# Kernel tuning notes

Hardware: AMD Instinct MI355X
Metric: run time of the kernel (lower is better)

## Reference

```python
import jax, jax.numpy as jnp
import numpy as np

N = 50000      # nodes
E = 800000     # edges (avg degree 16)
D = 128        # in_dim = hidden_dim
C = 40         # num_classes
BN_EPS = 1e-5


def setup_inputs() -> dict:
    key = jax.random.key(0)
    ks = jax.random.split(key, 24)
    h = jax.random.normal(ks[0], (N, D), dtype=jnp.float32)
    edge_src = jax.random.randint(ks[1], (E,), 0, N)
    edge_dst = jax.random.randint(ks[2], (E,), 0, N)
    mask = jnp.ones((E, 1), dtype=jnp.float32)  # adj_mask2_fixed (frozen)

    def lin_w(k, fi, fo):
        return jax.random.normal(k, (fi, fo), dtype=jnp.float32) / np.sqrt(fi).astype(np.float32)

    def lin_b(k, fo):
        return jax.random.normal(k, (fo,), dtype=jnp.float32) * 0.01

    dims = [(D, D), (D, D), (D, C)]  # last GIN layer -> num_classes
    out = {"h": h, "edge_src": edge_src, "edge_dst": edge_dst, "mask": mask}
    for i, (fi, fo) in enumerate(dims):
        out[f"w{i}"] = lin_w(ks[3 + 4 * i], fi, fo)
        out[f"b{i}"] = lin_b(ks[4 + 4 * i], fo)
        out[f"g{i}"] = jnp.ones((fo,), jnp.float32) + 0.05 * jax.random.normal(ks[5 + 4 * i], (fo,), jnp.float32)
        out[f"beta{i}"] = 0.05 * jax.random.normal(ks[6 + 4 * i], (fo,), jnp.float32)
        out[f"rm{i}"] = 0.1 * jax.random.normal(jax.random.fold_in(key, 100 + i), (fo,), jnp.float32)
        out[f"rv{i}"] = jax.random.uniform(jax.random.fold_in(key, 200 + i), (fo,), jnp.float32, 0.5, 1.5)
    out["wp"] = lin_w(ks[20], D, C)
    out["bp"] = lin_b(ks[21], C)
    return out


def reference(h, edge_src, edge_dst, mask,
              w0, b0, g0, beta0, rm0, rv0,
              w1, b1, g1, beta1, rm1, rv1,
              w2, b2, g2, beta2, rm2, rv2,
              wp, bp):
    # in-degree for mean aggregation (DGL mean reducer: divide by in-degree,
    # zero for isolated nodes)
    ones_e = jnp.ones(edge_dst.shape, dtype=h.dtype)
    deg = jax.ops.segment_sum(ones_e, edge_dst, num_segments=N)
    deg_inv = jnp.where(deg > 0, 1.0 / jnp.maximum(deg, 1.0), 0.0)[:, None]

    def gin_layer(x, w, b, g, beta, rm, rv):
        msg = x[edge_src] * mask                                   # [E, d]
        agg = jax.ops.segment_sum(msg, edge_dst, num_segments=N) * deg_inv
        z = (x + agg) @ w + b                                      # (1+eps)=1, eps=0
        z = (z - rm) * jax.lax.rsqrt(rv + BN_EPS) * g + beta       # BN (eval, running stats)
        return jax.nn.relu(z)                                      # dropout: eval -> identity

    h1 = gin_layer(h, w0, b0, g0, beta0, rm0, rv0)    # [N, D]
    h2 = gin_layer(h1, w1, b1, g1, beta1, rm1, rv1)   # [N, D]  hidden_rep[-2]
    h3 = gin_layer(h2, w2, b2, g2, beta2, rm2, rv2)   # [N, C]  hidden_rep[-1]
    return ((h2 @ wp + bp) + h3) * 0.5
```

## Files before the change

### kernel.cpp

```cpp
#include <hip/hip_runtime.h>

#define N_NODES 50000
#define N_EDGES 800000
#define DIM 128
#define NCLS 40

#define NCHUNK 128
#define CE 6250
#define HALF_N 25088
#define WHALF 12544
#define SCAN_B 98
#define N_PAD 50432

typedef __bf16 bf16x8_t __attribute__((ext_vector_type(8)));
typedef unsigned short us8_t __attribute__((ext_vector_type(8)));
typedef float f32x4_t __attribute__((ext_vector_type(4)));

static __device__ __forceinline__ float b2f(unsigned short h) {
    unsigned u = ((unsigned)h) << 16;
    return __builtin_bit_cast(float, u);
}
static __device__ __forceinline__ unsigned short f2b(float f) {
    unsigned u = __builtin_bit_cast(unsigned, f);
    u += 0x7FFFu + ((u >> 16) & 1u);
    return (unsigned short)(u >> 16);
}

__global__ __launch_bounds__(256) void to_bf16(const float* __restrict__ in,
                                               unsigned short* __restrict__ out) {
    size_t e0 = ((size_t)blockIdx.x * 256 + threadIdx.x) * 8;
    f32x4_t v0 = *(const f32x4_t*)(in + e0);
    f32x4_t v1 = *(const f32x4_t*)(in + e0 + 4);
    us8_t o;
    #pragma unroll
    for (int j = 0; j < 4; ++j) { o[j] = f2b(v0[j]); o[4 + j] = f2b(v1[j]); }
    *(us8_t*)(out + e0) = o;
}

__global__ __launch_bounds__(256) void repack_w(const float* __restrict__ w0,
                                                const float* __restrict__ w1,
                                                const float* __restrict__ w2,
                                                const float* __restrict__ wp,
                                                unsigned short* __restrict__ f0h,
                                                unsigned short* __restrict__ f0l,
                                                unsigned short* __restrict__ f1h,
                                                unsigned short* __restrict__ f1l,
                                                unsigned short* __restrict__ f2h,
                                                unsigned short* __restrict__ f2l,
                                                unsigned short* __restrict__ fph,
                                                unsigned short* __restrict__ fpl) {
    int t = blockIdx.x * 256 + threadIdx.x;
    const float* src;
    unsigned short *dh, *dl;
    int idx, ncols;
    if (t < 16384)      { src = w0; dh = f0h; dl = f0l; idx = t;         ncols = 128; }
    else if (t < 32768) { src = w1; dh = f1h; dl = f1l; idx = t - 16384; ncols = 128; }
    else if (t < 38912) { src = w2; dh = f2h; dl = f2l; idx = t - 32768; ncols = 48; }
    else if (t < 45056) { src = wp; dh = fph; dl = fpl; idx = t - 38912; ncols = 48; }
    else return;
    int k = idx / ncols, n = idx - k * ncols;
    float v;
    if (ncols == 128) v = src[k * 128 + n];
    else              v = (n < NCLS) ? src[k * NCLS + n] : 0.f;
    int nt = n >> 4, m = n & 15, kt = k >> 5, quad = (k >> 3) & 3, j = k & 7;
    int off = ((nt * 4 + kt) * 64 + quad * 16 + m) * 8 + j;
    unsigned short hi = f2b(v);
    dh[off] = hi;
    dl[off] = f2b(v - b2f(hi));
}

__global__ __launch_bounds__(256) void chunk_count(const int* __restrict__ dst,
                                                   unsigned* __restrict__ cnt) {
    __shared__ unsigned lds[WHALF];
    int c = blockIdx.x, h = blockIdx.y, tid = threadIdx.x;
    for (int w = tid; w < WHALF; w += 256) lds[w] = 0;
    __syncthreads();
    int base = c * CE;
    for (int k = tid; k < CE; k += 256) {
        int local = dst[base + k] - h * HALF_N;
        if (local >= 0 && local < HALF_N)
            atomicAdd(&lds[local >> 1], 1u << ((local & 1) * 16));
    }
    __syncthreads();
    unsigned* out = cnt + ((size_t)(h * NCHUNK + c)) * WHALF;
    for (int w = tid; w < WHALF; w += 256) out[w] = lds[w];
}

__global__ __launch_bounds__(256) void cscan(unsigned* __restrict__ cnt,
                                             unsigned* __restrict__ degp,
                                             int* __restrict__ partial) {
    __shared__ int lds[256];
    int b = blockIdx.x;
    int h = b / 49;
    int w = (b % 49) * 256 + threadIdx.x;
    unsigned acc = 0;
    for (int c = 0; c < NCHUNK; ++c) {
        size_t idx = ((size_t)(h * NCHUNK + c)) * WHALF + w;
        unsigned v = cnt[idx];
        cnt[idx] = acc;
        acc += v;
    }
    degp[h * WHALF + w] = acc;
    lds[threadIdx.x] = (int)(acc & 0xFFFFu) + (int)(acc >> 16);
    __syncthreads();
    #pragma unroll
    for (int off = 128; off > 0; off >>= 1) {
        if (threadIdx.x < off) lds[threadIdx.x] += lds[threadIdx.x + off];
        __syncthreads();
    }
    if (threadIdx.x == 0) partial[b] = lds[0];
}

__global__ __launch_bounds__(128) void scan_blocks(const int* __restrict__ partial,
                                                   int* __restrict__ blk_off) {
    __shared__ int lds[128];
    int tid = threadIdx.x;
    lds[tid] = (tid < SCAN_B) ? partial[tid] : 0;
    __syncthreads();
    #pragma unroll
    for (int off = 1; off < 128; off <<= 1) {
        int v = lds[tid];
        int add = (tid >= off) ? lds[tid - off] : 0;
        __syncthreads();
        lds[tid] = v + add;
        __syncthreads();
    }
    if (tid < SCAN_B) blk_off[tid] = (tid == 0) ? 0 : lds[tid - 1];
}

__global__ __launch_bounds__(256) void scan_final(const unsigned* __restrict__ degp,
                                                  const int* __restrict__ blk_off,
                                                  int* __restrict__ rs,
                                                  int* __restrict__ deg,
                                                  float* __restrict__ dinv) {
    __shared__ int lds[256];
    int b = blockIdx.x;
    int h = b / 49;
    int tid = threadIdx.x;
    int w = (b % 49) * 256 + tid;
    unsigned dp = degp[h * WHALF + w];
    int lo = (int)(dp & 0xFFFFu), hi = (int)(dp >> 16);
    int s = lo + hi;
    lds[tid] = s;
    __syncthreads();
    #pragma unroll
    for (int off = 1; off < 256; off <<= 1) {
        int v = lds[tid];
        int add = (tid >= off) ? lds[tid - off] : 0;
        __syncthreads();
        lds[tid] = v + add;
        __syncthreads();
    }
    int excl = blk_off[b] + lds[tid] - s;
    int n0 = h * HALF_N + 2 * w;
    rs[n0] = excl;
    rs[n0 + 1] = excl + lo;
    deg[n0] = lo;
    deg[n0 + 1] = hi;
    dinv[n0] = (lo > 0) ? (1.0f / (float)lo) : 0.0f;
    dinv[n0 + 1] = (hi > 0) ? (1.0f / (float)hi) : 0.0f;
}

__global__ __launch_bounds__(256) void fill2(const int* __restrict__ src,
                                             const int* __restrict__ dst,
                                             const float* __restrict__ mask,
                                             const unsigned* __restrict__ cnt,
                                             const int* __restrict__ rs,
                                             unsigned* __restrict__ csr) {
    __shared__ unsigned cur[WHALF];
    int c = blockIdx.x, h = blockIdx.y, tid = threadIdx.x;
    const unsigned* off = cnt + ((size_t)(h * NCHUNK + c)) * WHALF;
    for (int w = tid; w < WHALF; w += 256) cur[w] = off[w];
    __syncthreads();
    int base = c * CE;
    for (int k = tid; k < CE; k += 256) {
        int e = base + k;
        int d = dst[e];
        int local = d - h * HALF_N;
        if (local >= 0 && local < HALF_N) {
            unsigned sm = (unsigned)src[e] | ((unsigned)f2b(mask[e]) << 16);
            int sh = (local & 1) * 16;
            unsigned old = atomicAdd(&cur[local >> 1], 1u << sh);
            int rank = (int)((old >> sh) & 0xFFFFu);
            csr[rs[d] + rank] = sm;
        }
    }
}

__global__ __launch_bounds__(256) void agg_kernel(const unsigned short* __restrict__ xb,
                                                  const float* __restrict__ x,
                                                  float* __restrict__ xin,
                                                  const int* __restrict__ rs,
                                                  const int* __restrict__ deg,
                                                  const float* __restrict__ dinv,
                                                  const unsigned* __restrict__ csr) {
    int lane = threadIdx.x & 63;
    int node = blockIdx.x * 4 + (threadIdx.x >> 6);
    if (node >= N_NODES) return;
    int cnt = deg[node];
    int start = rs[node];
    float acc0 = 0.f, acc1 = 0.f;
    for (int base = 0; base < cnt; base += 16) {
        int nb = cnt - base;
        if (nb > 16) nb = 16;
        unsigned pk = 0;
        if (lane < nb) pk = csr[start + base + lane];
        unsigned vv[16];
        float mm[16];
        #pragma unroll
        for (int j = 0; j < 16; ++j) {
            unsigned p = (unsigned)__builtin_amdgcn_readlane((int)pk, j);
            mm[j] = b2f((unsigned short)(p >> 16));
            vv[j] = *(const unsigned*)(xb + (size_t)(p & 0xFFFFu) * DIM + lane * 2);
        }
        #pragma unroll
        for (int j = 0; j < 16; ++j) {
            acc0 += mm[j] * b2f((unsigned short)(vv[j] & 0xFFFFu));
            acc1 += mm[j] * b2f((unsigned short)(vv[j] >> 16));
        }
    }
    float di = dinv[node];
    float2 xp = *(const float2*)(x + (size_t)node * DIM + lane * 2);
    float2 o;
    o.x = xp.x + acc0 * di;
    o.y = xp.y + acc1 * di;
    *(float2*)(xin + (size_t)node * DIM + lane * 2) = o;
}

__global__ __launch_bounds__(256) void gemm128_bn_relu(const float* __restrict__ xin,
                                                       const unsigned short* __restrict__ wfh,
                                                       const unsigned short* __restrict__ wfl,
                                                       const float* __restrict__ bias,
                                                       const float* __restrict__ gam,
                                                       const float* __restrict__ bet,
                                                       const float* __restrict__ rm,
                                                       const float* __restrict__ rv,
                                                       float* __restrict__ out,
                                                       unsigned short* __restrict__ outb) {
    int tid = threadIdx.x;
    int wave = tid >> 6, lane = tid & 63;
    int m = lane & 15, quad = lane >> 4;
    int rbase = blockIdx.x * 64 + wave * 16;
    int arow = rbase + m;
    const float* ap = xin + (size_t)(arow < N_NODES ? arow : 0) * DIM;

    us8_t ah[4], al[4];
    #pragma unroll
    for (int kt = 0; kt < 4; ++kt) {
        f32x4_t p0 = *(const f32x4_t*)(ap + kt * 32 + quad * 8);
        f32x4_t p1 = *(const f32x4_t*)(ap + kt * 32 + quad * 8 + 4);
        #pragma unroll
        for (int j = 0; j < 4; ++j) {
            unsigned short h0 = f2b(p0[j]);
            unsigned short h1 = f2b(p1[j]);
            ah[kt][j] = h0;
            ah[kt][4 + j] = h1;
            al[kt][j] = f2b(p0[j] - b2f(h0));
            al[kt][4 + j] = f2b(p1[j] - b2f(h1));
        }
    }

    f32x4_t acc[8] = {};
    #pragma unroll
    for (int kt = 0; kt < 4; ++kt) {
        #pragma unroll
        for (int nt = 0; nt < 8; ++nt) {
            int boff = ((nt * 4 + kt) * 64 + lane) * 8;
            us8_t bh = *(const us8_t*)(wfh + boff);
            us8_t bl = *(const us8_t*)(wfl + boff);
            acc[nt] = __builtin_amdgcn_mfma_f32_16x16x32_bf16(
                __builtin_bit_cast(bf16x8_t, ah[kt]),
                __builtin_bit_cast(bf16x8_t, bh), acc[nt], 0, 0, 0);
            acc[nt] = __builtin_amdgcn_mfma_f32_16x16x32_bf16(
                __builtin_bit_cast(bf16x8_t, ah[kt]),
                __builtin_bit_cast(bf16x8_t, bl), acc[nt], 0, 0, 0);
            acc[nt] = __builtin_amdgcn_mfma_f32_16x16x32_bf16(
                __builtin_bit_cast(bf16x8_t, al[kt]),
                __builtin_bit_cast(bf16x8_t, bh), acc[nt], 0, 0, 0);
        }
    }

    #pragma unroll
    for (int nt = 0; nt < 8; ++nt) {
        int j = nt * 16 + m;
        float bj = bias[j];
        float sc = gam[j] * rsqrtf(rv[j] + 1e-5f);
        float sh = bet[j] - rm[j] * sc;
        #pragma unroll
        for (int i = 0; i < 4; ++i) {
            int r = rbase + quad * 4 + i;
            if (r < N_NODES) {
                float z = fmaxf((acc[nt][i] + bj) * sc + sh, 0.f);
                out[(size_t)r * DIM + j] = z;
                outb[(size_t)r * DIM + j] = f2b(z);
            }
        }
    }
}

__global__ __launch_bounds__(256) void fused_final(const float* __restrict__ xin2,
                                                   const float* __restrict__ h2,
                                                   const unsigned short* __restrict__ f2h,
                                                   const unsigned short* __restrict__ f2l,
                                                   const unsigned short* __restrict__ fph,
                                                   const unsigned short* __restrict__ fpl,
                                                   const float* __restrict__ b2,
                                                   const float* __restrict__ g2,
                                                   const float* __restrict__ be2,
                                                   const float* __restrict__ rm2,
                                                   const float* __restrict__ rv2,
                                                   const float* __restrict__ bp,
                                                   float* __restrict__ out) {
    int tid = threadIdx.x;
    int wave = tid >> 6, lane = tid & 63;
    int m = lane & 15, quad = lane >> 4;
    int rbase = blockIdx.x * 64 + wave * 16;
    int arow = rbase + m;
    size_t rowoff = (size_t)(arow < N_NODES ? arow : 0) * DIM;
    const float* ap2 = xin2 + rowoff;
    const float* aph = h2 + rowoff;

    us8_t a2h[4], a2l[4], ahh[4], ahl[4];
    #pragma unroll
    for (int kt = 0; kt < 4; ++kt) {
        f32x4_t p0 = *(const f32x4_t*)(ap2 + kt * 32 + quad * 8);
        f32x4_t p1 = *(const f32x4_t*)(ap2 + kt * 32 + quad * 8 + 4);
        f32x4_t q0 = *(const f32x4_t*)(aph + kt * 32 + quad * 8);
        f32x4_t q1 = *(const f32x4_t*)(aph + kt * 32 + quad * 8 + 4);
        #pragma unroll
        for (int j = 0; j < 4; ++j) {
            unsigned short h0 = f2b(p0[j]), h1 = f2b(p1[j]);
            a2h[kt][j] = h0; a2h[kt][4 + j] = h1;
            a2l[kt][j] = f2b(p0[j] - b2f(h0));
            a2l[kt][4 + j] = f2b(p1[j] - b2f(h1));
            unsigned short g0 = f2b(q0[j]), g1 = f2b(q1[j]);
            ahh[kt][j] = g0; ahh[kt][4 + j] = g1;
            ahl[kt][j] = f2b(q0[j] - b2f(g0));
            ahl[kt][4 + j] = f2b(q1[j] - b2f(g1));
        }
    }

    f32x4_t acc2[3] = {};
    f32x4_t accp[3] = {};
    #pragma unroll
    for (int kt = 0; kt < 4; ++kt) {
        #pragma unroll
        for (int nt = 0; nt < 3; ++nt) {
            int boff = ((nt * 4 + kt) * 64 + lane) * 8;
            us8_t b2hv = *(const us8_t*)(f2h + boff);
            us8_t b2lv = *(const us8_t*)(f2l + boff);
            us8_t bphv = *(const us8_t*)(fph + boff);
            us8_t bplv = *(const us8_t*)(fpl + boff);
            acc2[nt] = __builtin_amdgcn_mfma_f32_16x16x32_bf16(
                __builtin_bit_cast(bf16x8_t, a2h[kt]),
                __builtin_bit_cast(bf16x8_t, b2hv), acc2[nt], 0, 0, 0);
            acc2[nt] = __builtin_amdgcn_mfma_f32_16x16x32_bf16(
                __builtin_bit_cast(bf16x8_t, a2h[kt]),
                __builtin_bit_cast(bf16x8_t, b2lv), acc2[nt], 0, 0, 0);
            acc2[nt] = __builtin_amdgcn_mfma_f32_16x16x32_bf16(
                __builtin_bit_cast(bf16x8_t, a2l[kt]),
                __builtin_bit_cast(bf16x8_t, b2hv), acc2[nt], 0, 0, 0);
            accp[nt] = __builtin_amdgcn_mfma_f32_16x16x32_bf16(
                __builtin_bit_cast(bf16x8_t, ahh[kt]),
                __builtin_bit_cast(bf16x8_t, bphv), accp[nt], 0, 0, 0);
            accp[nt] = __builtin_amdgcn_mfma_f32_16x16x32_bf16(
                __builtin_bit_cast(bf16x8_t, ahh[kt]),
                __builtin_bit_cast(bf16x8_t, bplv), accp[nt], 0, 0, 0);
            accp[nt] = __builtin_amdgcn_mfma_f32_16x16x32_bf16(
                __builtin_bit_cast(bf16x8_t, ahl[kt]),
                __builtin_bit_cast(bf16x8_t, bphv), accp[nt], 0, 0, 0);
        }
    }

    #pragma unroll
    for (int nt = 0; nt < 3; ++nt) {
        int j = nt * 16 + m;
        int jc = (j < NCLS) ? j : (NCLS - 1);
        float b2j = b2[jc];
        float sc = g2[jc] * rsqrtf(rv2[jc] + 1e-5f);
        float sh = be2[jc] - rm2[jc] * sc;
        float bpj = bp[jc];
        #pragma unroll
        for (int i = 0; i < 4; ++i) {
            int r = rbase + quad * 4 + i;
            if (r < N_NODES && j < NCLS) {
                float z = fmaxf((acc2[nt][i] + b2j) * sc + sh, 0.f);
                float p = accp[nt][i] + bpj;
                out[(size_t)r * NCLS + j] = (p + z) * 0.5f;
            }
        }
    }
}

extern "C" void kernel_launch(void* const* d_in, const int* in_sizes, int n_in,
                              void* d_out, int out_size, void* d_ws, size_t ws_size,
                              hipStream_t stream) {
    const float* h    = (const float*)d_in[0];
    const int* esrc   = (const int*)d_in[1];
    const int* edst   = (const int*)d_in[2];
    const float* mask = (const float*)d_in[3];
    const float* w0   = (const float*)d_in[4];
    const float* b0   = (const float*)d_in[5];
    const float* g0   = (const float*)d_in[6];
    const float* be0  = (const float*)d_in[7];
    const float* rm0  = (const float*)d_in[8];
    const float* rv0  = (const float*)d_in[9];
    const float* w1   = (const float*)d_in[10];
    const float* b1   = (const float*)d_in[11];
    const float* g1   = (const float*)d_in[12];
    const float* be1  = (const float*)d_in[13];
    const float* rm1  = (const float*)d_in[14];
    const float* rv1  = (const float*)d_in[15];
    const float* w2   = (const float*)d_in[16];
    const float* b2   = (const float*)d_in[17];
    const float* g2   = (const float*)d_in[18];
    const float* be2  = (const float*)d_in[19];
    const float* rm2  = (const float*)d_in[20];
    const float* rv2  = (const float*)d_in[21];
    const float* wp   = (const float*)d_in[22];
    const float* bp   = (const float*)d_in[23];

    char* ws = (char*)d_ws;
    size_t off = 0;
    auto alloc = [&](size_t bytes) {
        char* p = ws + off;
        off = (off + bytes + 255) & ~(size_t)255;
        return p;
    };
    int* rs       = (int*)alloc(N_PAD * 4);
    int* deg      = (int*)alloc(N_PAD * 4);
    float* dinv   = (float*)alloc(N_PAD * 4);
    int* partial  = (int*)alloc(128 * 4);
    int* blk_off  = (int*)alloc(128 * 4);
    unsigned* degp = (unsigned*)alloc(2 * WHALF * 4);
    unsigned* csr = (unsigned*)alloc((size_t)N_EDGES * 4);
    float* xin    = (float*)alloc((size_t)N_NODES * DIM * 4);
    float* hb     = (float*)alloc((size_t)N_NODES * DIM * 4);
    unsigned short* xb16 = (unsigned short*)alloc((size_t)N_NODES * DIM * 2);
    unsigned short* hb16 = (unsigned short*)alloc((size_t)N_NODES * DIM * 2);
    unsigned short* f0h = (unsigned short*)alloc(16384 * 2);
    unsigned short* f0l = (unsigned short*)alloc(16384 * 2);
    unsigned short* f1h = (unsigned short*)alloc(16384 * 2);
    unsigned short* f1l = (unsigned short*)alloc(16384 * 2);
    unsigned short* f2h = (unsigned short*)alloc(6144 * 2);
    unsigned short* f2l = (unsigned short*)alloc(6144 * 2);
    unsigned short* fph = (unsigned short*)alloc(6144 * 2);
    unsigned short* fpl = (unsigned short*)alloc(6144 * 2);
    unsigned* cnt = (unsigned*)xin;

    const int AB = (N_NODES + 3) / 4;
    const int GB = (N_NODES + 63) / 64;

    to_bf16<<<3125, 256, 0, stream>>>(h, xb16);
    repack_w<<<176, 256, 0, stream>>>(w0, w1, w2, wp, f0h, f0l, f1h, f1l,
                                      f2h, f2l, fph, fpl);
    chunk_count<<<dim3(NCHUNK, 2), 256, 0, stream>>>(edst, cnt);
    cscan<<<SCAN_B, 256, 0, stream>>>(cnt, degp, partial);
    scan_blocks<<<1, 128, 0, stream>>>(partial, blk_off);
    scan_final<<<SCAN_B, 256, 0, stream>>>(degp, blk_off, rs, deg, dinv);
    fill2<<<dim3(NCHUNK, 2), 256, 0, stream>>>(esrc, edst, mask, cnt, rs, csr);

    agg_kernel<<<AB, 256, 0, stream>>>(xb16, h, xin, rs, deg, dinv, csr);
    gemm128_bn_relu<<<GB, 256, 0, stream>>>(xin, f0h, f0l, b0, g0, be0, rm0, rv0, hb, hb16);
    agg_kernel<<<AB, 256, 0, stream>>>(hb16, hb, xin, rs, deg, dinv, csr);
    gemm128_bn_relu<<<GB, 256, 0, stream>>>(xin, f1h, f1l, b1, g1, be1, rm1, rv1, hb, hb16);
    agg_kernel<<<AB, 256, 0, stream>>>(hb16, hb, xin, rs, deg, dinv, csr);
    fused_final<<<GB, 256, 0, stream>>>(xin, hb, f2h, f2l, fph, fpl,
                                        b2, g2, be2, rm2, rv2, bp, (float*)d_out);
}
```

Before: 338.7 us.

## Fuse neighbor aggregation into the GEMM+BN+ReLU kernels via LDS staging

```diff
diff --git a/kernel.cpp b/kernel.cpp
--- a/kernel.cpp
+++ b/kernel.cpp
@@ -187,19 +187,10 @@
     }
 }
 
-__global__ __launch_bounds__(256) void agg_kernel(const unsigned short* __restrict__ xb,
-                                                  const float* __restrict__ x,
-                                                  float* __restrict__ xin,
-                                                  const int* __restrict__ rs,
-                                                  const int* __restrict__ deg,
-                                                  const float* __restrict__ dinv,
-                                                  const unsigned* __restrict__ csr) {
-    int lane = threadIdx.x & 63;
-    int node = blockIdx.x * 4 + (threadIdx.x >> 6);
-    if (node >= N_NODES) return;
-    int cnt = deg[node];
-    int start = rs[node];
-    float acc0 = 0.f, acc1 = 0.f;
+static __device__ __forceinline__ void gather_node(const unsigned short* __restrict__ xb,
+                                                   const unsigned* __restrict__ csr,
+                                                   int start, int cnt, int lane,
+                                                   float& acc0, float& acc1) {
     for (int base = 0; base < cnt; base += 16) {
         int nb = cnt - base;
         if (nb > 16) nb = 16;
@@ -219,30 +210,45 @@
             acc1 += mm[j] * b2f((unsigned short)(vv[j] >> 16));
         }
     }
-    float di = dinv[node];
-    float2 xp = *(const float2*)(x + (size_t)node * DIM + lane * 2);
-    float2 o;
-    o.x = xp.x + acc0 * di;
-    o.y = xp.y + acc1 * di;
-    *(float2*)(xin + (size_t)node * DIM + lane * 2) = o;
-}
-
-__global__ __launch_bounds__(256) void gemm128_bn_relu(const float* __restrict__ xin,
-                                                       const unsigned short* __restrict__ wfh,
-                                                       const unsigned short* __restrict__ wfl,
-                                                       const float* __restrict__ bias,
-                                                       const float* __restrict__ gam,
-                                                       const float* __restrict__ bet,
-                                                       const float* __restrict__ rm,
-                                                       const float* __restrict__ rv,
-                                                       float* __restrict__ out,
-                                                       unsigned short* __restrict__ outb) {
+}
+
+__global__ __launch_bounds__(256) void fused_layer(const unsigned short* __restrict__ xb,
+                                                   const float* __restrict__ x,
+                                                   const int* __restrict__ rs,
+                                                   const int* __restrict__ deg,
+                                                   const float* __restrict__ dinv,
+                                                   const unsigned* __restrict__ csr,
+                                                   const unsigned short* __restrict__ wfh,
+                                                   const unsigned short* __restrict__ wfl,
+                                                   const float* __restrict__ bias,
+                                                   const float* __restrict__ gam,
+                                                   const float* __restrict__ bet,
+                                                   const float* __restrict__ rm,
+                                                   const float* __restrict__ rv,
+                                                   float* __restrict__ out,
+                                                   unsigned short* __restrict__ outb) {
+    __shared__ float lds[4][16][132];
     int tid = threadIdx.x;
     int wave = tid >> 6, lane = tid & 63;
+    int rbase = blockIdx.x * 64 + wave * 16;
+
+    for (int i = 0; i < 16; ++i) {
+        int node = rbase + i;
+        float acc0 = 0.f, acc1 = 0.f;
+        if (node < N_NODES) {
+            gather_node(xb, csr, rs[node], deg[node], lane, acc0, acc1);
+            float di = dinv[node];
+            float2 xp = *(const float2*)(x + (size_t)node * DIM + lane * 2);
+            acc0 = xp.x + acc0 * di;
+            acc1 = xp.y + acc1 * di;
+        }
+        lds[wave][i][lane * 2] = acc0;
+        lds[wave][i][lane * 2 + 1] = acc1;
+    }
+    __syncthreads();
+
     int m = lane & 15, quad = lane >> 4;
-    int rbase = blockIdx.x * 64 + wave * 16;
-    int arow = rbase + m;
-    const float* ap = xin + (size_t)(arow < N_NODES ? arow : 0) * DIM;
+    const float* ap = &lds[wave][m][0];
 
     us8_t ah[4], al[4];
     #pragma unroll
@@ -298,27 +304,47 @@
     }
 }
 
-__global__ __launch_bounds__(256) void fused_final(const float* __restrict__ xin2,
-                                                   const float* __restrict__ h2,
-                                                   const unsigned short* __restrict__ f2h,
-                                                   const unsigned short* __restrict__ f2l,
-                                                   const unsigned short* __restrict__ fph,
-                                                   const unsigned short* __restrict__ fpl,
-                                                   const float* __restrict__ b2,
-                                                   const float* __restrict__ g2,
-                                                   const float* __restrict__ be2,
-                                                   const float* __restrict__ rm2,
-                                                   const float* __restrict__ rv2,
-                                                   const float* __restrict__ bp,
-                                                   float* __restrict__ out) {
+__global__ __launch_bounds__(256) void fused_final2(const unsigned short* __restrict__ xb,
+                                                    const float* __restrict__ h2,
+                                                    const int* __restrict__ rs,
+                                                    const int* __restrict__ deg,
+                                                    const float* __restrict__ dinv,
+                                                    const unsigned* __restrict__ csr,
+                                                    const unsigned short* __restrict__ f2h,
+                                                    const unsigned short* __restrict__ f2l,
+                                                    const unsigned short* __restrict__ fph,
+                                                    const unsigned short* __restrict__ fpl,
+                                                    const float* __restrict__ b2,
+                                                    const float* __restrict__ g2,
+                                                    const float* __restrict__ be2,
+                                                    const float* __restrict__ rm2,
+                                                    const float* __restrict__ rv2,
+                                                    const float* __restrict__ bp,
+                                                    float* __restrict__ out) {
+    __shared__ float lds[4][16][132];
     int tid = threadIdx.x;
     int wave = tid >> 6, lane = tid & 63;
+    int rbase = blockIdx.x * 64 + wave * 16;
+
+    for (int i = 0; i < 16; ++i) {
+        int node = rbase + i;
+        float acc0 = 0.f, acc1 = 0.f;
+        if (node < N_NODES) {
+            gather_node(xb, csr, rs[node], deg[node], lane, acc0, acc1);
+            float di = dinv[node];
+            float2 xp = *(const float2*)(h2 + (size_t)node * DIM + lane * 2);
+            acc0 = xp.x + acc0 * di;
+            acc1 = xp.y + acc1 * di;
+        }
+        lds[wave][i][lane * 2] = acc0;
+        lds[wave][i][lane * 2 + 1] = acc1;
+    }
+    __syncthreads();
+
     int m = lane & 15, quad = lane >> 4;
-    int rbase = blockIdx.x * 64 + wave * 16;
     int arow = rbase + m;
-    size_t rowoff = (size_t)(arow < N_NODES ? arow : 0) * DIM;
-    const float* ap2 = xin2 + rowoff;
-    const float* aph = h2 + rowoff;
+    const float* ap2 = &lds[wave][m][0];
+    const float* aph = h2 + (size_t)(arow < N_NODES ? arow : 0) * DIM;
 
     us8_t a2h[4], a2l[4], ahh[4], ahl[4];
     #pragma unroll
@@ -434,10 +460,12 @@
     int* blk_off  = (int*)alloc(128 * 4);
     unsigned* degp = (unsigned*)alloc(2 * WHALF * 4);
     unsigned* csr = (unsigned*)alloc((size_t)N_EDGES * 4);
-    float* xin    = (float*)alloc((size_t)N_NODES * DIM * 4);
-    float* hb     = (float*)alloc((size_t)N_NODES * DIM * 4);
-    unsigned short* xb16 = (unsigned short*)alloc((size_t)N_NODES * DIM * 2);
-    unsigned short* hb16 = (unsigned short*)alloc((size_t)N_NODES * DIM * 2);
+    unsigned* cnt = (unsigned*)alloc((size_t)2 * NCHUNK * WHALF * 4);
+    float* hbA    = (float*)alloc((size_t)N_NODES * DIM * 4);
+    float* hbB    = (float*)alloc((size_t)N_NODES * DIM * 4);
+    unsigned short* xb16  = (unsigned short*)alloc((size_t)N_NODES * DIM * 2);
+    unsigned short* hbA16 = (unsigned short*)alloc((size_t)N_NODES * DIM * 2);
+    unsigned short* hbB16 = (unsigned short*)alloc((size_t)N_NODES * DIM * 2);
     unsigned short* f0h = (unsigned short*)alloc(16384 * 2);
     unsigned short* f0l = (unsigned short*)alloc(16384 * 2);
     unsigned short* f1h = (unsigned short*)alloc(16384 * 2);
@@ -446,9 +474,7 @@
     unsigned short* f2l = (unsigned short*)alloc(6144 * 2);
     unsigned short* fph = (unsigned short*)alloc(6144 * 2);
     unsigned short* fpl = (unsigned short*)alloc(6144 * 2);
-    unsigned* cnt = (unsigned*)xin;
-
-    const int AB = (N_NODES + 3) / 4;
+
     const int GB = (N_NODES + 63) / 64;
 
     to_bf16<<<3125, 256, 0, stream>>>(h, xb16);
@@ -460,11 +486,11 @@
     scan_final<<<SCAN_B, 256, 0, stream>>>(degp, blk_off, rs, deg, dinv);
     fill2<<<dim3(NCHUNK, 2), 256, 0, stream>>>(esrc, edst, mask, cnt, rs, csr);
 
-    agg_kernel<<<AB, 256, 0, stream>>>(xb16, h, xin, rs, deg, dinv, csr);
-    gemm128_bn_relu<<<GB, 256, 0, stream>>>(xin, f0h, f0l, b0, g0, be0, rm0, rv0, hb, hb16);
-    agg_kernel<<<AB, 256, 0, stream>>>(hb16, hb, xin, rs, deg, dinv, csr);
-    gemm128_bn_relu<<<GB, 256, 0, stream>>>(xin, f1h, f1l, b1, g1, be1, rm1, rv1, hb, hb16);
-    agg_kernel<<<AB, 256, 0, stream>>>(hb16, hb, xin, rs, deg, dinv, csr);
-    fused_final<<<GB, 256, 0, stream>>>(xin, hb, f2h, f2l, fph, fpl,
-                                        b2, g2, be2, rm2, rv2, bp, (float*)d_out);
-}
+    fused_layer<<<GB, 256, 0, stream>>>(xb16, h, rs, deg, dinv, csr,
+                                        f0h, f0l, b0, g0, be0, rm0, rv0, hbA, hbA16);
+    fused_layer<<<GB, 256, 0, stream>>>(hbA16, hbA, rs, deg, dinv, csr,
+                                        f1h, f1l, b1, g1, be1, rm1, rv1, hbB, hbB16);
+    fused_final2<<<GB, 256, 0, stream>>>(hbB16, hbB, rs, deg, dinv, csr,
+                                         f2h, f2l, fph, fpl,
+                                         b2, g2, be2, rm2, rv2, bp, (float*)d_out);
+}
```

After: 369.1 us. 9.0% more time.
